# Performance work log

Measured on AMD Instinct MI355X. Metric: run time of the kernel, lower is better.

Reference implementation:

```python
import jax, jax.numpy as jnp
import numpy as np

B, N, DIM, H = 4, 4096, 1024, 16
HD = DIM // H  # head dim = 64


def setup_inputs() -> dict:
    key = jax.random.key(0)
    ks = jax.random.split(key, 12)
    s = 1.0 / np.sqrt(DIM)
    return {
        "query": jax.random.normal(ks[0], (B, N, DIM), jnp.float32),
        "key": jax.random.normal(ks[1], (B, N, DIM), jnp.float32),
        "value": jax.random.normal(ks[2], (B, N, DIM), jnp.float32),
        "Wq": jax.random.uniform(ks[3], (DIM, DIM), jnp.float32, -s, s),
        "bq": jax.random.uniform(ks[4], (DIM,), jnp.float32, -s, s),
        "Wk": jax.random.uniform(ks[5], (DIM, DIM), jnp.float32, -s, s),
        "bk": jax.random.uniform(ks[6], (DIM,), jnp.float32, -s, s),
        "Wv": jax.random.uniform(ks[7], (DIM, DIM), jnp.float32, -s, s),
        "bv": jax.random.uniform(ks[8], (DIM,), jnp.float32, -s, s),
        "Wo": jax.random.uniform(ks[9], (DIM, DIM), jnp.float32, -s, s),
        "bo": jax.random.uniform(ks[10], (DIM,), jnp.float32, -s, s),
        "key_padding_mask": jax.random.randint(ks[11], (B, N), 0, 2) == 1,
        "need_weights": 0,
    }


def reference(query, key, value, Wq, bq, Wk, bk, Wv, bv, Wo, bo, key_padding_mask, need_weights):
    h = H
    q = jax.nn.relu(query @ Wq.T + bq)            # [b,n,dim]
    k = jax.nn.relu(key @ Wk.T + bk)
    v = value @ Wv.T + bv
    # zero out padded keys
    k = jnp.where(key_padding_mask[:, :, None], 0.0, k)
    b, n, d = q.shape
    q = q.reshape(b, n, h, d // h)                # [b,n,h,hd]
    k = k.reshape(b, n, h, d // h)
    v = v.reshape(b, n, h, d // h)
    kv = jnp.einsum("bnhd,bnhe->bhde", k, v)      # [b,h,hd,hd]
    denom = 1.0 / (jnp.einsum("bnhd,bhd->bnh", q, k.sum(axis=1)) + 1e-6)
    out = jnp.einsum("bnhd,bhde->bnhe", q, kv) * denom[..., None]
    out = out.reshape(b, n, d)
    return out @ Wo.T + bo
```

## Files before the change

### kernel.cpp

```cpp
#include <hip/hip_runtime.h>
#include <hip/hip_bf16.h>
#include <stdint.h>

#define DIM   1024
#define NSEQ  4096
#define NBAT  4
#define NH    16
#define HD    64
#define MROWS (NBAT*NSEQ)

typedef __attribute__((ext_vector_type(8))) short  short8;
typedef __attribute__((ext_vector_type(4))) float  f32x4;
typedef __attribute__((ext_vector_type(4))) unsigned int  u32x4;
typedef __attribute__((ext_vector_type(4))) unsigned short u16x4;
typedef __attribute__((ext_vector_type(8))) unsigned short u16x8;

__device__ inline unsigned short bf16_rne(float x) {
    unsigned u = __builtin_bit_cast(unsigned, x);
    u += 0x7FFFu + ((u >> 16) & 1u);
    return (unsigned short)(u >> 16);
}
__device__ inline float bf16_to_f32(unsigned short h) {
    return __builtin_bit_cast(float, ((unsigned)h) << 16);
}
__device__ inline u16x8 cvt8(f32x4 a, f32x4 b) {
    u16x8 o;
    o[0] = bf16_rne(a[0]); o[1] = bf16_rne(a[1]); o[2] = bf16_rne(a[2]); o[3] = bf16_rne(a[3]);
    o[4] = bf16_rne(b[0]); o[5] = bf16_rne(b[1]); o[6] = bf16_rne(b[2]); o[7] = bf16_rne(b[3]);
    return o;
}
__device__ inline void gld16(const unsigned short* g, unsigned short* l) {
    __builtin_amdgcn_global_load_lds(
        (const __attribute__((address_space(1))) unsigned int*)g,
        (__attribute__((address_space(3))) unsigned int*)l,
        16, 0, 0);
}

__global__ __launch_bounds__(256) void wcvt_kernel(const float* __restrict__ s0, const float* __restrict__ s1,
                                                   const float* __restrict__ s2, const float* __restrict__ s3,
                                                   unsigned short* __restrict__ d0, unsigned short* __restrict__ d1,
                                                   unsigned short* __restrict__ d2, unsigned short* __restrict__ d3) {
    int i = blockIdx.x * 256 + threadIdx.x;
    int w = i >> 17, j = i & 131071;
    const float* s = (w == 0) ? s0 : (w == 1) ? s1 : (w == 2) ? s2 : s3;
    unsigned short* d = (w == 0) ? d0 : (w == 1) ? d1 : (w == 2) ? d2 : d3;
    f32x4 a = ((const f32x4*)s)[2 * j];
    f32x4 b = ((const f32x4*)s)[2 * j + 1];
    ((u16x8*)d)[j] = cvt8(a, b);
}

__global__ __launch_bounds__(256) void acvt2_kernel(const float* __restrict__ s0, const float* __restrict__ s1,
                                                    unsigned short* __restrict__ d0, unsigned short* __restrict__ d1) {
    const int b = blockIdx.x & 4095, w = blockIdx.x >> 12;
    const float* s = w ? s1 : s0;
    unsigned short* d = w ? d1 : d0;
    const int t0 = b * 256 + (int)threadIdx.x;
    const int c0 = t0, c1 = t0 + 1048576;
    const f32x4* sp = (const f32x4*)s;
    f32x4 x0 = sp[2 * c0], x1 = sp[2 * c0 + 1];
    f32x4 y0 = sp[2 * c1], y1 = sp[2 * c1 + 1];
    ((u16x8*)d)[c0] = cvt8(x0, x1);
    ((u16x8*)d)[c1] = cvt8(y0, y1);
}
__global__ __launch_bounds__(256) void acvt1_kernel(const float* __restrict__ s0, unsigned short* __restrict__ d0) {
    const int t0 = blockIdx.x * 256 + (int)threadIdx.x;
    const int c0 = t0, c1 = t0 + 1048576;
    const f32x4* sp = (const f32x4*)s0;
    f32x4 x0 = sp[2 * c0], x1 = sp[2 * c0 + 1];
    f32x4 y0 = sp[2 * c1], y1 = sp[2 * c1 + 1];
    ((u16x8*)d0)[c0] = cvt8(x0, x1);
    ((u16x8*)d0)[c1] = cvt8(y0, y1);
}

template<int ACT, int OUTF32>
__global__ __launch_bounds__(512, 2) void gemm8_kernel(const unsigned short* __restrict__ Ab,
                                                       const unsigned short* __restrict__ Wb,
                                                       const float* __restrict__ bias,
                                                       void* __restrict__ Cp,
                                                       const int* __restrict__ mask) {
    __shared__ __align__(16) char smem[131072];

    const int bid = blockIdx.x;
    const int swz = (bid & 7) * 32 + (bid >> 3);
    const int tm  = (swz >> 2) * 256;
    const int tn  = (swz & 3) * 256;

    const int t    = threadIdx.x;
    const int w    = t >> 6;
    const int lane = t & 63;
    const int wm   = w >> 2;
    const int wn   = w & 3;
    const int lm   = lane & 15;
    const int quad = lane >> 4;

    const int xr    = ((quad ^ ((lm >> 1) & 3)) << 4) + (lm & 1) * 64;
    const int abase = (wm * 64 + (lm >> 1)) * 128 + xr;
    const int bbase = (wn * 32 + (lm >> 1)) * 128 + xr;

    const int srow = ((t >> 3) << 1) + ((t >> 2) & 1);
    const int scol = ((t & 3) ^ ((t >> 3) & 3)) * 8;
    const unsigned short* pa = Ab + (size_t)(tm + srow) * DIM + scol;
    const unsigned short* pb = Wb + (size_t)(tn + srow) * DIM + scol;

    f32x4 acc[8][4] = {};
    const int NT = DIM / 32;

#pragma unroll
    for (int pt = 0; pt < 3; ++pt) {
        char* dst = smem + pt * 16384;
        gld16(pa + pt * 32,             (unsigned short*)(dst + t * 16));
        gld16(pa + 128 * DIM + pt * 32, (unsigned short*)(dst + 8192 + t * 16));
        gld16(pb + pt * 32,             (unsigned short*)(dst + 65536 + t * 16));
        gld16(pb + 128 * DIM + pt * 32, (unsigned short*)(dst + 65536 + 8192 + t * 16));
        __builtin_amdgcn_sched_barrier(0);
    }
    asm volatile("s_waitcnt vmcnt(8)" ::: "memory");
    __builtin_amdgcn_s_barrier();
    __builtin_amdgcn_sched_barrier(0);

    short8 bf[4];
    for (int kt = 0; kt < NT; ++kt) {
        const int  slot = (kt & 3) * 16384;
        const int  ks   = (kt + 3 < NT) ? kt + 3 : NT - 1;
        char*      stg  = smem + ((kt + 3) & 3) * 16384;

        gld16(pa + ks * 32,             (unsigned short*)(stg + t * 16));
        gld16(pa + 128 * DIM + ks * 32, (unsigned short*)(stg + 8192 + t * 16));
        short8 af[4];
#pragma unroll
        for (int i = 0; i < 4; ++i)
            af[i] = *(const short8*)(smem + slot + abase + i * 1024);
#pragma unroll
        for (int j = 0; j < 4; ++j)
            bf[j] = *(const short8*)(smem + slot + 65536 + bbase + j * 1024);
        __builtin_amdgcn_s_barrier();
        asm volatile("s_waitcnt lgkmcnt(0)" ::: "memory");
        __builtin_amdgcn_sched_barrier(0);
        __builtin_amdgcn_s_setprio(1);
#pragma unroll
        for (int i = 0; i < 4; ++i)
#pragma unroll
            for (int j = 0; j < 4; ++j)
                acc[i][j] = __builtin_amdgcn_mfma_f32_16x16x32_bf16(af[i], bf[j], acc[i][j], 0, 0, 0);
        __builtin_amdgcn_s_setprio(0);
        __builtin_amdgcn_s_barrier();
        __builtin_amdgcn_sched_barrier(0);

        gld16(pb + ks * 32,             (unsigned short*)(stg + 65536 + t * 16));
        gld16(pb + 128 * DIM + ks * 32, (unsigned short*)(stg + 65536 + 8192 + t * 16));
#pragma unroll
        for (int i = 0; i < 4; ++i)
            af[i] = *(const short8*)(smem + slot + abase + 4096 + i * 1024);
        __builtin_amdgcn_s_barrier();
        asm volatile("s_waitcnt lgkmcnt(0)" ::: "memory");
        __builtin_amdgcn_sched_barrier(0);
        __builtin_amdgcn_s_setprio(1);
#pragma unroll
        for (int i = 0; i < 4; ++i)
#pragma unroll
            for (int j = 0; j < 4; ++j)
                acc[i + 4][j] = __builtin_amdgcn_mfma_f32_16x16x32_bf16(af[i], bf[j], acc[i + 4][j], 0, 0, 0);
        __builtin_amdgcn_s_setprio(0);
        asm volatile("s_waitcnt vmcnt(8)" ::: "memory");
        __builtin_amdgcn_s_barrier();
        __builtin_amdgcn_sched_barrier(0);
    }

    asm volatile("s_waitcnt vmcnt(0)" ::: "memory");

    const int crow0 = tm + wm * 128 + quad * 4;
    const int ccol0 = tn + wn * 64 + lm;
#pragma unroll
    for (int i = 0; i < 8; ++i) {
#pragma unroll
        for (int r = 0; r < 4; ++r) {
            const int row = crow0 + i * 16 + r;
            int mz = 0;
            if constexpr (ACT == 2) mz = mask[row];
#pragma unroll
            for (int j = 0; j < 4; ++j) {
                const int col = ccol0 + j * 16;
                float v = acc[i][j][r] + bias[col];
                if constexpr (ACT >= 1) v = v > 0.f ? v : 0.f;
                if constexpr (ACT == 2) { if (mz) v = 0.f; }
                if constexpr (OUTF32)
                    ((float*)Cp)[(size_t)row * DIM + col] = v;
                else
                    ((unsigned short*)Cp)[(size_t)row * DIM + col] = bf16_rne(v);
            }
        }
    }
}

__device__ inline int rowoff(int d) { return d * 40 + ((d >> 3) & 1) * 8; }

__global__ __launch_bounds__(256) void kvmfma_kernel(const unsigned short* __restrict__ kb,
                                                     const unsigned short* __restrict__ vb,
                                                     float* __restrict__ kvT8,
                                                     float* __restrict__ ksum8) {
    __shared__ unsigned short kT[2624];
    __shared__ unsigned short vT[2624];
    __shared__ float ksl[64];

    const int bh    = blockIdx.x;
    const int bb    = bh >> 4, h = bh & 15;
    const int chunk = blockIdx.y;
    const int t     = threadIdx.x;
    const int w     = t >> 6;
    const int lane  = t & 63;
    const int lm    = lane & 15;
    const int quad  = lane >> 4;
    const int sn    = t >> 3;
    const int d0    = (t & 7) * 8;

    const size_t gbase = ((size_t)bb * NSEQ + (size_t)chunk * 512) * DIM + h * HD;
    const unsigned short* kp = kb + gbase + (size_t)sn * DIM + d0;
    const unsigned short* vp = vb + gbase + (size_t)sn * DIM + d0;

    if (t < 64) ksl[t] = 0.f;

    float ks[8] = {};
    f32x4 acc[4] = {};

    for (int n0 = 0; n0 < 512; n0 += 32) {
        short8 kx = *(const short8*)(kp + (size_t)n0 * DIM);
        short8 vx = *(const short8*)(vp + (size_t)n0 * DIM);
        __syncthreads();
#pragma unroll
        for (int j = 0; j < 8; ++j) {
            const int ro = rowoff(d0 + j);
            kT[ro + sn] = (unsigned short)kx[j];
            vT[ro + sn] = (unsigned short)vx[j];
            ks[j] += bf16_to_f32((unsigned short)kx[j]);
        }
        __syncthreads();
        short8 afrag = *(const short8*)(vT + rowoff(w * 16 + lm) + quad * 8);
#pragma unroll
        for (int jd = 0; jd < 4; ++jd) {
            short8 bfrag = *(const short8*)(kT + rowoff(jd * 16 + lm) + quad * 8);
            acc[jd] = __builtin_amdgcn_mfma_f32_16x16x32_bf16(afrag, bfrag, acc[jd], 0, 0, 0);
        }
    }

    const size_t obase = ((size_t)chunk * 64 + bh) * 4096;
#pragma unroll
    for (int jd = 0; jd < 4; ++jd)
#pragma unroll
        for (int r = 0; r < 4; ++r) {
            const int e = w * 16 + quad * 4 + r;
            const int d = jd * 16 + lm;
            kvT8[obase + e * 64 + d] = acc[jd][r];
        }

    __syncthreads();
#pragma unroll
    for (int j = 0; j < 8; ++j) atomicAdd(&ksl[d0 + j], ks[j]);
    __syncthreads();
    if (t < 64) ksum8[((size_t)chunk * 64 + bh) * 64 + t] = ksl[t];
}

__global__ __launch_bounds__(256) void kvsum_kernel(const float* __restrict__ kvT8,
                                                    const float* __restrict__ ksum8,
                                                    unsigned short* __restrict__ kvTb,
                                                    float* __restrict__ ksum) {
    int idx = blockIdx.x * 256 + threadIdx.x;
    if (idx < 262144) {
        float s = 0.f;
#pragma unroll
        for (int c = 0; c < 8; ++c) s += kvT8[(size_t)c * 262144 + idx];
        kvTb[idx] = bf16_rne(s);
    } else {
        int j = idx - 262144;
        float s = 0.f;
#pragma unroll
        for (int c = 0; c < 8; ++c) s += ksum8[(size_t)c * 4096 + j];
        ksum[j] = s;
    }
}

__global__ __launch_bounds__(256) void attnout_kernel(const unsigned short* __restrict__ qb,
                                                      const unsigned short* __restrict__ kvTb,
                                                      const float* __restrict__ ksum,
                                                      unsigned short* __restrict__ attn) {
    const int n0   = blockIdx.x * 16;
    const int bb   = n0 >> 12;
    const int t    = threadIdx.x;
    const int w    = t >> 6;
    const int lane = t & 63;
    const int lm   = lane & 15;
    const int quad = lane >> 4;

    for (int hh = 0; hh < 4; ++hh) {
        const int h  = w * 4 + hh;
        const int bh = bb * NH + h;
        const unsigned short* qp = qb + (size_t)(n0 + lm) * DIM + h * HD + quad * 8;
        short8 a0 = *(const short8*)qp;
        short8 a1 = *(const short8*)(qp + 32);

        const float* ksp = ksum + (size_t)bh * HD + quad * 8;
        float part = 0.f;
#pragma unroll
        for (int j = 0; j < 8; ++j)
            part += bf16_to_f32((unsigned short)a0[j]) * ksp[j]
                  + bf16_to_f32((unsigned short)a1[j]) * ksp[32 + j];
        part += __shfl_xor(part, 16, 64);
        part += __shfl_xor(part, 32, 64);
        float dinv = 1.f / (part + 1e-6f);

        f32x4 accs[4];
#pragma unroll
        for (int j = 0; j < 4; ++j) {
            const unsigned short* bp = kvTb + ((size_t)bh * HD + j * 16 + lm) * HD + quad * 8;
            short8 b0 = *(const short8*)bp;
            short8 b1 = *(const short8*)(bp + 32);
            f32x4 c = {};
            c = __builtin_amdgcn_mfma_f32_16x16x32_bf16(a0, b0, c, 0, 0, 0);
            c = __builtin_amdgcn_mfma_f32_16x16x32_bf16(a1, b1, c, 0, 0, 0);
            accs[j] = c;
        }
        float dv[4];
#pragma unroll
        for (int r = 0; r < 4; ++r)
            dv[r] = __shfl(dinv, quad * 4 + r, 64);
#pragma unroll
        for (int j = 0; j < 4; ++j)
#pragma unroll
            for (int r = 0; r < 4; ++r) {
                const int row = n0 + quad * 4 + r;
                attn[(size_t)row * DIM + h * HD + j * 16 + lm] = bf16_rne(accs[j][r] * dv[r]);
            }
    }
}

extern "C" void kernel_launch(void* const* d_in, const int* in_sizes, int n_in,
                              void* d_out, int out_size, void* d_ws, size_t ws_size,
                              hipStream_t stream) {
    const float* query = (const float*)d_in[0];
    const float* key   = (const float*)d_in[1];
    const float* value = (const float*)d_in[2];
    const float* Wq    = (const float*)d_in[3];
    const float* bq    = (const float*)d_in[4];
    const float* Wk    = (const float*)d_in[5];
    const float* bk    = (const float*)d_in[6];
    const float* Wv    = (const float*)d_in[7];
    const float* bv    = (const float*)d_in[8];
    const float* Wo    = (const float*)d_in[9];
    const float* bo    = (const float*)d_in[10];
    const int*   mask  = (const int*)d_in[11];
    float* out = (float*)d_out;
    char*  ws  = (char*)d_ws;
    const size_t MB = 1024ull * 1024ull;

    unsigned short* Wqb  = (unsigned short*)(ws + 0 * MB);
    unsigned short* Wkb  = (unsigned short*)(ws + 2 * MB);
    unsigned short* Wvb  = (unsigned short*)(ws + 4 * MB);
    unsigned short* Wob  = (unsigned short*)(ws + 6 * MB);
    unsigned short* qb   = (unsigned short*)(ws + 8 * MB);
    unsigned short* kb   = (unsigned short*)(ws + 40 * MB);
    unsigned short* kvTb = (unsigned short*)(ws + 72 * MB);
    float*          ksum = (float*)(ws + 73 * MB);
    unsigned short* attn = kb;

    unsigned short* Qbf   = (unsigned short*)d_out;
    unsigned short* Kbf   = (unsigned short*)((char*)d_out + 32 * MB);
    unsigned short* Vbf   = Kbf;
    unsigned short* vb    = (unsigned short*)d_out;
    float*          kvT8  = (float*)((char*)d_out + 32 * MB);
    float*          ksum8 = (float*)((char*)d_out + 40 * MB);

    wcvt_kernel<<<2048, 256, 0, stream>>>(Wq, Wk, Wv, Wo, Wqb, Wkb, Wvb, Wob);
    acvt2_kernel<<<8192, 256, 0, stream>>>(query, key, Qbf, Kbf);

    gemm8_kernel<1, 0><<<256, 512, 0, stream>>>(Qbf, Wqb, bq, qb, nullptr);
    gemm8_kernel<2, 0><<<256, 512, 0, stream>>>(Kbf, Wkb, bk, kb, mask);
    acvt1_kernel<<<4096, 256, 0, stream>>>(value, Vbf);
    gemm8_kernel<0, 0><<<256, 512, 0, stream>>>(Vbf, Wvb, bv, vb, nullptr);

    kvmfma_kernel<<<dim3(64, 8), 256, 0, stream>>>(kb, vb, kvT8, ksum8);
    kvsum_kernel<<<1040, 256, 0, stream>>>(kvT8, ksum8, kvTb, ksum);
    attnout_kernel<<<1024, 256, 0, stream>>>(qb, kvTb, ksum, attn);

    gemm8_kernel<0, 1><<<256, 512, 0, stream>>>(attn, Wob, bo, out, nullptr);
}
```

Measured before the change: 440.6 us.

## Fuse fp32-to-bf16 activation conversion into the Q/K/V projection GEMMs

Removes the separate activation conversion kernels. A new GEMM variant loads fp32 activations straight into registers two k-tiles ahead, packs them to bf16 with v_cvt_pk_bf16_f32 and writes them to LDS, while weights still arrive through direct global-to-LDS loads. This avoids writing and re-reading 96MB of bf16 intermediates. In exchange the A loads go through VGPRs, which adds register pressure and extra ALU and LDS-store work inside the pipelined loop.

```diff
diff --git a/kernel.cpp b/kernel.cpp
--- a/kernel.cpp
+++ b/kernel.cpp
@@ -12,7 +12,6 @@
 typedef __attribute__((ext_vector_type(8))) short  short8;
 typedef __attribute__((ext_vector_type(4))) float  f32x4;
 typedef __attribute__((ext_vector_type(4))) unsigned int  u32x4;
-typedef __attribute__((ext_vector_type(4))) unsigned short u16x4;
 typedef __attribute__((ext_vector_type(8))) unsigned short u16x8;
 
 __device__ inline unsigned short bf16_rne(float x) {
@@ -49,35 +48,15 @@
     ((u16x8*)d)[j] = cvt8(a, b);
 }
 
-__global__ __launch_bounds__(256) void acvt2_kernel(const float* __restrict__ s0, const float* __restrict__ s1,
-                                                    unsigned short* __restrict__ d0, unsigned short* __restrict__ d1) {
-    const int b = blockIdx.x & 4095, w = blockIdx.x >> 12;
-    const float* s = w ? s1 : s0;
-    unsigned short* d = w ? d1 : d0;
-    const int t0 = b * 256 + (int)threadIdx.x;
-    const int c0 = t0, c1 = t0 + 1048576;
-    const f32x4* sp = (const f32x4*)s;
-    f32x4 x0 = sp[2 * c0], x1 = sp[2 * c0 + 1];
-    f32x4 y0 = sp[2 * c1], y1 = sp[2 * c1 + 1];
-    ((u16x8*)d)[c0] = cvt8(x0, x1);
-    ((u16x8*)d)[c1] = cvt8(y0, y1);
-}
-__global__ __launch_bounds__(256) void acvt1_kernel(const float* __restrict__ s0, unsigned short* __restrict__ d0) {
-    const int t0 = blockIdx.x * 256 + (int)threadIdx.x;
-    const int c0 = t0, c1 = t0 + 1048576;
-    const f32x4* sp = (const f32x4*)s0;
-    f32x4 x0 = sp[2 * c0], x1 = sp[2 * c0 + 1];
-    f32x4 y0 = sp[2 * c1], y1 = sp[2 * c1 + 1];
-    ((u16x8*)d0)[c0] = cvt8(x0, x1);
-    ((u16x8*)d0)[c1] = cvt8(y0, y1);
-}
-
-template<int ACT, int OUTF32>
-__global__ __launch_bounds__(512, 2) void gemm8_kernel(const unsigned short* __restrict__ Ab,
-                                                       const unsigned short* __restrict__ Wb,
-                                                       const float* __restrict__ bias,
-                                                       void* __restrict__ Cp,
-                                                       const int* __restrict__ mask) {
+#define SB0 __builtin_amdgcn_sched_barrier(0)
+#define MF(i, j, A, B) acc[i][j] = __builtin_amdgcn_mfma_f32_16x16x32_bf16(A, B, acc[i][j], 0, 0, 0)
+
+template<int ACT>
+__global__ __launch_bounds__(512, 2) void gemm8a32_kernel(const float* __restrict__ Af,
+                                                          const unsigned short* __restrict__ Wb,
+                                                          const float* __restrict__ bias,
+                                                          unsigned short* __restrict__ Cp,
+                                                          const int* __restrict__ mask) {
     __shared__ __align__(16) char smem[131072];
 
     const int bid = blockIdx.x;
@@ -99,6 +78,145 @@
 
     const int srow = ((t >> 3) << 1) + ((t >> 2) & 1);
     const int scol = ((t & 3) ^ ((t >> 3) & 3)) * 8;
+    const float*          pa = Af + (size_t)(tm + srow) * DIM + scol;
+    const unsigned short* pb = Wb + (size_t)(tn + srow) * DIM + scol;
+
+    f32x4 acc[8][4] = {};
+    const int NT = DIM / 32;
+
+#define ALOAD(k, r0, r1, r2, r3) do {                          \
+    r0 = *(const f32x4*)(pa + (k) * 32);                       \
+    r1 = *(const f32x4*)(pa + (k) * 32 + 4);                   \
+    r2 = *(const f32x4*)(pa + (k) * 32 + 128 * DIM);           \
+    r3 = *(const f32x4*)(pa + (k) * 32 + 128 * DIM + 4); } while (0)
+#define BSTAGE(k, sl) do {                                                    \
+    char* dstb = smem + 65536 + (sl) * 16384;                                 \
+    gld16(pb + (k) * 32,             (unsigned short*)(dstb + t * 16));       \
+    gld16(pb + (k) * 32 + 128 * DIM, (unsigned short*)(dstb + 8192 + t * 16)); } while (0)
+#define APACK(sl, r0, r1, r2, r3) do {                                           \
+    unsigned w0, w1, w2, w3, w4, w5, w6, w7;                                     \
+    asm("v_cvt_pk_bf16_f32 %0, %1, %2" : "=v"(w0) : "v"(r0[0]), "v"(r0[1]));     \
+    asm("v_cvt_pk_bf16_f32 %0, %1, %2" : "=v"(w1) : "v"(r0[2]), "v"(r0[3]));     \
+    asm("v_cvt_pk_bf16_f32 %0, %1, %2" : "=v"(w2) : "v"(r1[0]), "v"(r1[1]));     \
+    asm("v_cvt_pk_bf16_f32 %0, %1, %2" : "=v"(w3) : "v"(r1[2]), "v"(r1[3]));     \
+    asm("v_cvt_pk_bf16_f32 %0, %1, %2" : "=v"(w4) : "v"(r2[0]), "v"(r2[1]));     \
+    asm("v_cvt_pk_bf16_f32 %0, %1, %2" : "=v"(w5) : "v"(r2[2]), "v"(r2[3]));     \
+    asm("v_cvt_pk_bf16_f32 %0, %1, %2" : "=v"(w6) : "v"(r3[0]), "v"(r3[1]));     \
+    asm("v_cvt_pk_bf16_f32 %0, %1, %2" : "=v"(w7) : "v"(r3[2]), "v"(r3[3]));     \
+    char* sa = smem + (sl) * 16384;                                              \
+    u32x4 d0v = {w0, w1, w2, w3}, d1v = {w4, w5, w6, w7};                        \
+    *(u32x4*)(sa + t * 16) = d0v;                                                \
+    *(u32x4*)(sa + 8192 + t * 16) = d1v; } while (0)
+
+#define ITER(kt, R0, R1, R2, R3, N0, N1, N2, N3) do {                            \
+    const int ksa  = ((kt) + 2 < NT) ? (kt) + 2 : NT - 1;                        \
+    const int ksb  = ((kt) + 3 < NT) ? (kt) + 3 : NT - 1;                        \
+    const int slot = ((kt) & 3) * 16384;                                         \
+    ALOAD(ksa, N0, N1, N2, N3); SB0;                                             \
+    BSTAGE(ksb, ((kt) + 3) & 3); SB0;                                            \
+    short8 af0 = *(const short8*)(smem + slot + abase);                          \
+    short8 af1 = *(const short8*)(smem + slot + abase + 1024);                   \
+    short8 af2 = *(const short8*)(smem + slot + abase + 2048);                   \
+    short8 af3 = *(const short8*)(smem + slot + abase + 3072);                   \
+    short8 bf0 = *(const short8*)(smem + slot + 65536 + bbase);                  \
+    short8 bf1 = *(const short8*)(smem + slot + 65536 + bbase + 1024);           \
+    short8 bf2 = *(const short8*)(smem + slot + 65536 + bbase + 2048);           \
+    short8 bf3 = *(const short8*)(smem + slot + 65536 + bbase + 3072);           \
+    __builtin_amdgcn_s_barrier();                                                \
+    asm volatile("s_waitcnt lgkmcnt(0)" ::: "memory");                           \
+    SB0;                                                                         \
+    __builtin_amdgcn_s_setprio(1);                                               \
+    MF(0,0,af0,bf0); MF(0,1,af0,bf1); MF(0,2,af0,bf2); MF(0,3,af0,bf3);          \
+    MF(1,0,af1,bf0); MF(1,1,af1,bf1); MF(1,2,af1,bf2); MF(1,3,af1,bf3);          \
+    MF(2,0,af2,bf0); MF(2,1,af2,bf1); MF(2,2,af2,bf2); MF(2,3,af2,bf3);          \
+    MF(3,0,af3,bf0); MF(3,1,af3,bf1); MF(3,2,af3,bf2); MF(3,3,af3,bf3);          \
+    __builtin_amdgcn_s_setprio(0);                                               \
+    __builtin_amdgcn_s_barrier(); SB0;                                           \
+    asm volatile("s_waitcnt vmcnt(8)" ::: "memory"); SB0;                        \
+    APACK(((kt) + 1) & 3, R0, R1, R2, R3);                                       \
+    short8 ag0 = *(const short8*)(smem + slot + abase + 4096);                   \
+    short8 ag1 = *(const short8*)(smem + slot + abase + 4096 + 1024);            \
+    short8 ag2 = *(const short8*)(smem + slot + abase + 4096 + 2048);            \
+    short8 ag3 = *(const short8*)(smem + slot + abase + 4096 + 3072);            \
+    __builtin_amdgcn_s_barrier();                                                \
+    asm volatile("s_waitcnt lgkmcnt(0)" ::: "memory");                           \
+    SB0;                                                                         \
+    __builtin_amdgcn_s_setprio(1);                                               \
+    MF(4,0,ag0,bf0); MF(4,1,ag0,bf1); MF(4,2,ag0,bf2); MF(4,3,ag0,bf3);          \
+    MF(5,0,ag1,bf0); MF(5,1,ag1,bf1); MF(5,2,ag1,bf2); MF(5,3,ag1,bf3);          \
+    MF(6,0,ag2,bf0); MF(6,1,ag2,bf1); MF(6,2,ag2,bf2); MF(6,3,ag2,bf3);          \
+    MF(7,0,ag3,bf0); MF(7,1,ag3,bf1); MF(7,2,ag3,bf2); MF(7,3,ag3,bf3);          \
+    __builtin_amdgcn_s_setprio(0);                                               \
+    __builtin_amdgcn_s_barrier(); SB0; } while (0)
+
+    f32x4 c0, c1, c2, c3, n0, n1, n2, n3;
+    ALOAD(0, c0, c1, c2, c3); SB0;
+    BSTAGE(0, 0); SB0;
+    ALOAD(1, n0, n1, n2, n3); SB0;
+    BSTAGE(1, 1); BSTAGE(2, 2); SB0;
+    asm volatile("s_waitcnt vmcnt(8)" ::: "memory");
+    APACK(0, c0, c1, c2, c3);
+    asm volatile("s_waitcnt lgkmcnt(0)" ::: "memory");
+    __builtin_amdgcn_s_barrier();
+    SB0;
+
+    for (int kt = 0; kt < NT; kt += 2) {
+        ITER(kt,     n0, n1, n2, n3, c0, c1, c2, c3);
+        ITER(kt + 1, c0, c1, c2, c3, n0, n1, n2, n3);
+    }
+
+    asm volatile("s_waitcnt vmcnt(0) lgkmcnt(0)" ::: "memory");
+
+    const int crow0 = tm + wm * 128 + quad * 4;
+    const int ccol0 = tn + wn * 64 + lm;
+#pragma unroll
+    for (int i = 0; i < 8; ++i) {
+#pragma unroll
+        for (int r = 0; r < 4; ++r) {
+            const int row = crow0 + i * 16 + r;
+            int mz = 0;
+            if constexpr (ACT == 2) mz = mask[row];
+#pragma unroll
+            for (int j = 0; j < 4; ++j) {
+                const int col = ccol0 + j * 16;
+                float v = acc[i][j][r] + bias[col];
+                if constexpr (ACT >= 1) v = v > 0.f ? v : 0.f;
+                if constexpr (ACT == 2) { if (mz) v = 0.f; }
+                Cp[(size_t)row * DIM + col] = bf16_rne(v);
+            }
+        }
+    }
+#undef ITER
+#undef APACK
+#undef BSTAGE
+#undef ALOAD
+}
+
+__global__ __launch_bounds__(512, 2) void gemm8_kernel(const unsigned short* __restrict__ Ab,
+                                                       const unsigned short* __restrict__ Wb,
+                                                       const float* __restrict__ bias,
+                                                       float* __restrict__ Cp) {
+    __shared__ __align__(16) char smem[131072];
+
+    const int bid = blockIdx.x;
+    const int swz = (bid & 7) * 32 + (bid >> 3);
+    const int tm  = (swz >> 2) * 256;
+    const int tn  = (swz & 3) * 256;
+
+    const int t    = threadIdx.x;
+    const int w    = t >> 6;
+    const int lane = t & 63;
+    const int wm   = w >> 2;
+    const int wn   = w & 3;
+    const int lm   = lane & 15;
+    const int quad = lane >> 4;
+
+    const int xr    = ((quad ^ ((lm >> 1) & 3)) << 4) + (lm & 1) * 64;
+    const int abase = (wm * 64 + (lm >> 1)) * 128 + xr;
+    const int bbase = (wn * 32 + (lm >> 1)) * 128 + xr;
+
+    const int srow = ((t >> 3) << 1) + ((t >> 2) & 1);
+    const int scol = ((t & 3) ^ ((t >> 3) & 3)) * 8;
     const unsigned short* pa = Ab + (size_t)(tm + srow) * DIM + scol;
     const unsigned short* pb = Wb + (size_t)(tn + srow) * DIM + scol;
 
@@ -116,7 +234,7 @@
     }
     asm volatile("s_waitcnt vmcnt(8)" ::: "memory");
     __builtin_amdgcn_s_barrier();
-    __builtin_amdgcn_sched_barrier(0);
+    SB0;
 
     short8 bf[4];
     for (int kt = 0; kt < NT; ++kt) {
@@ -135,7 +253,7 @@
             bf[j] = *(const short8*)(smem + slot + 65536 + bbase + j * 1024);
         __builtin_amdgcn_s_barrier();
         asm volatile("s_waitcnt lgkmcnt(0)" ::: "memory");
-        __builtin_amdgcn_sched_barrier(0);
+        SB0;
         __builtin_amdgcn_s_setprio(1);
 #pragma unroll
         for (int i = 0; i < 4; ++i)
@@ -144,7 +262,7 @@
                 acc[i][j] = __builtin_amdgcn_mfma_f32_16x16x32_bf16(af[i], bf[j], acc[i][j], 0, 0, 0);
         __builtin_amdgcn_s_setprio(0);
         __builtin_amdgcn_s_barrier();
-        __builtin_amdgcn_sched_barrier(0);
+        SB0;
 
         gld16(pb + ks * 32,             (unsigned short*)(stg + 65536 + t * 16));
         gld16(pb + 128 * DIM + ks * 32, (unsigned short*)(stg + 65536 + 8192 + t * 16));
@@ -153,7 +271,7 @@
             af[i] = *(const short8*)(smem + slot + abase + 4096 + i * 1024);
         __builtin_amdgcn_s_barrier();
         asm volatile("s_waitcnt lgkmcnt(0)" ::: "memory");
-        __builtin_amdgcn_sched_barrier(0);
+        SB0;
         __builtin_amdgcn_s_setprio(1);
 #pragma unroll
         for (int i = 0; i < 4; ++i)
@@ -163,7 +281,7 @@
         __builtin_amdgcn_s_setprio(0);
         asm volatile("s_waitcnt vmcnt(8)" ::: "memory");
         __builtin_amdgcn_s_barrier();
-        __builtin_amdgcn_sched_barrier(0);
+        SB0;
     }
 
     asm volatile("s_waitcnt vmcnt(0)" ::: "memory");
@@ -171,25 +289,15 @@
     const int crow0 = tm + wm * 128 + quad * 4;
     const int ccol0 = tn + wn * 64 + lm;
 #pragma unroll
-    for (int i = 0; i < 8; ++i) {
-#pragma unroll
-        for (int r = 0; r < 4; ++r) {
-            const int row = crow0 + i * 16 + r;
-            int mz = 0;
-            if constexpr (ACT == 2) mz = mask[row];
+    for (int i = 0; i < 8; ++i)
+#pragma unroll
+        for (int r = 0; r < 4; ++r)
 #pragma unroll
             for (int j = 0; j < 4; ++j) {
+                const int row = crow0 + i * 16 + r;
                 const int col = ccol0 + j * 16;
-                float v = acc[i][j][r] + bias[col];
-                if constexpr (ACT >= 1) v = v > 0.f ? v : 0.f;
-                if constexpr (ACT == 2) { if (mz) v = 0.f; }
-                if constexpr (OUTF32)
-                    ((float*)Cp)[(size_t)row * DIM + col] = v;
-                else
-                    ((unsigned short*)Cp)[(size_t)row * DIM + col] = bf16_rne(v);
+                Cp[(size_t)row * DIM + col] = acc[i][j][r] + bias[col];
             }
-        }
-    }
 }
 
 __device__ inline int rowoff(int d) { return d * 40 + ((d >> 3) & 1) * 8; }
@@ -361,24 +469,19 @@
     float*          ksum = (float*)(ws + 73 * MB);
     unsigned short* attn = kb;
 
-    unsigned short* Qbf   = (unsigned short*)d_out;
-    unsigned short* Kbf   = (unsigned short*)((char*)d_out + 32 * MB);
-    unsigned short* Vbf   = Kbf;
     unsigned short* vb    = (unsigned short*)d_out;
     float*          kvT8  = (float*)((char*)d_out + 32 * MB);
     float*          ksum8 = (float*)((char*)d_out + 40 * MB);
 
     wcvt_kernel<<<2048, 256, 0, stream>>>(Wq, Wk, Wv, Wo, Wqb, Wkb, Wvb, Wob);
-    acvt2_kernel<<<8192, 256, 0, stream>>>(query, key, Qbf, Kbf);
-
-    gemm8_kernel<1, 0><<<256, 512, 0, stream>>>(Qbf, Wqb, bq, qb, nullptr);
-    gemm8_kernel<2, 0><<<256, 512, 0, stream>>>(Kbf, Wkb, bk, kb, mask);
-    acvt1_kernel<<<4096, 256, 0, stream>>>(value, Vbf);
-    gemm8_kernel<0, 0><<<256, 512, 0, stream>>>(Vbf, Wvb, bv, vb, nullptr);
+
+    gemm8a32_kernel<1><<<256, 512, 0, stream>>>(query, Wqb, bq, qb, nullptr);
+    gemm8a32_kernel<2><<<256, 512, 0, stream>>>(key,   Wkb, bk, kb, mask);
+    gemm8a32_kernel<0><<<256, 512, 0, stream>>>(value, Wvb, bv, vb, nullptr);
 
     kvmfma_kernel<<<dim3(64, 8), 256, 0, stream>>>(kb, vb, kvT8, ksum8);
     kvsum_kernel<<<1040, 256, 0, stream>>>(kvT8, ksum8, kvTb, ksum);
     attnout_kernel<<<1024, 256, 0, stream>>>(qb, kvTb, ksum, attn);
 
-    gemm8_kernel<0, 1><<<256, 512, 0, stream>>>(attn, Wob, bo, out, nullptr);
-}
+    gemm8_kernel<<<256, 512, 0, stream>>>(attn, Wob, bo, out);
+}
```

Result: slower. 453.8 us (+3.0%).
